# Performance work log

Measured on AMD Instinct MI355X. Metric: run time of the kernel, lower is better.

Reference implementation:

```python
import jax, jax.numpy as jnp
import numpy as np

DIM = 128
HEADS = 4
DH = 32
SCALE = DH ** -0.5


def _ln(x, g, b):
    m = x.mean(-1, keepdims=True)
    v = x.var(-1, keepdims=True)
    return (x - m) / jnp.sqrt(v + 1e-5) * g + b


def setup_inputs() -> dict:
    key = jax.random.key(0)
    ks = jax.random.split(key, 16)
    B, N, H, W, HK, WK = 2, 6, 48, 48, 24, 24
    d, hd = DIM, HEADS * DH
    p = lambda k, s: (jax.random.normal(k, s, jnp.float32) * 0.02)
    return {
        "q": jax.random.normal(ks[0], (B, N, d, H, W), jnp.float32),
        "k": jax.random.normal(ks[1], (B, N, d, HK, WK), jnp.float32),
        "v": jax.random.normal(ks[2], (B, N, d, HK, WK), jnp.float32),
        "skip": jax.random.normal(ks[3], (B, d, H, W), jnp.float32),
        "lnq_g": jnp.ones(d), "lnq_b": jnp.zeros(d),
        "Wq": p(ks[4], (d, hd)), "bq": jnp.zeros(hd),
        "lnk_g": jnp.ones(d), "lnk_b": jnp.zeros(d),
        "Wk": p(ks[5], (d, hd)), "bk": jnp.zeros(hd),
        "lnv_g": jnp.ones(d), "lnv_b": jnp.zeros(d),
        "Wv": p(ks[6], (d, hd)), "bv": jnp.zeros(hd),
        "Wp": p(ks[7], (hd, d)), "bp": jnp.zeros(d),
        "pre_g": jnp.ones(d), "pre_b": jnp.zeros(d),
        "W1": p(ks[8], (d, 2 * d)), "b1": jnp.zeros(2 * d),
        "W2": p(ks[9], (2 * d, d)), "b2": jnp.zeros(d),
        "post_g": jnp.ones(d), "post_b": jnp.zeros(d),
    }


def reference(q, k, v, skip, lnq_g, lnq_b, Wq, bq, lnk_g, lnk_b, Wk, bk,
              lnv_g, lnv_b, Wv, bv, Wp, bp, pre_g, pre_b, W1, b1, W2, b2,
              post_g, post_b):
    B, N, d, H, W = q.shape
    _, _, _, HK, WK = k.shape
    Q, K = H * W, HK * WK
    # b n d H W -> b n (H W) d
    qx = q.transpose(0, 1, 3, 4, 2).reshape(B, N, Q, d)
    kx = k.transpose(0, 1, 3, 4, 2).reshape(B, N, K, d)
    vx = v.transpose(0, 1, 3, 4, 2).reshape(B, N * K, d)
    # norm + linear projections
    qp = _ln(qx, lnq_g, lnq_b) @ Wq + bq  # (B,N,Q,HEADS*DH)
    kp = _ln(kx, lnk_g, lnk_b) @ Wk + bk
    vp = _ln(vx, lnv_g, lnv_b) @ Wv + bv  # (B,N*K,HEADS*DH)
    # split heads: b ... (m d) -> (b m) ... d
    qp = qp.reshape(B, N, Q, HEADS, DH).transpose(0, 3, 1, 2, 4).reshape(B * HEADS, N, Q, DH)
    kp = kp.reshape(B, N, K, HEADS, DH).transpose(0, 3, 1, 2, 4).reshape(B * HEADS, N, K, DH)
    vp = vp.reshape(B, N * K, HEADS, DH).transpose(0, 2, 1, 3).reshape(B * HEADS, N * K, DH)
    # per-view scores, then softmax jointly over (n K)
    scores = SCALE * jnp.einsum('bnqd,bnkd->bnqk', qp, kp)
    scores = scores.transpose(0, 2, 1, 3).reshape(B * HEADS, Q, N * K)
    a = jax.nn.softmax(scores, axis=-1)
    out = jnp.einsum('bqk,bkd->bqd', a, vp)  # (B*HEADS, Q, DH)
    # merge heads: (b m) Q d -> b Q (m d)
    z = out.reshape(B, HEADS, Q, DH).transpose(0, 2, 1, 3).reshape(B, Q, HEADS * DH)
    z = z @ Wp + bp
    z = z + skip.transpose(0, 2, 3, 1).reshape(B, Q, d)
    z = _ln(z, pre_g, pre_b)
    z = z + (jax.nn.gelu(z @ W1 + b1, approximate=False) @ W2 + b2)
    z = _ln(z, post_g, post_b)
    return z.reshape(B, H, W, d).transpose(0, 3, 1, 2)
```

## Files before the change

### kernel.cpp

```cpp
#include <hip/hip_runtime.h>
#include <cmath>

#define B_    2
#define N_    6
#define D_    128
#define Q_    2304
#define K_    576
#define NK_   3456
#define HEADS_ 4
#define DH_   32
#define SCALE_ 0.17677669529663687f

typedef __attribute__((ext_vector_type(8))) short bf16x8;
typedef __attribute__((ext_vector_type(4))) float f32x4;

#if defined(__has_builtin)
#if __has_builtin(__builtin_amdgcn_cvt_pk_bf16_f32)
#define HAS_PK_BF16 1
#endif
#endif

static __device__ __forceinline__ unsigned short f2bf(float f) {
  union { float f; unsigned u; } x; x.f = f;
  unsigned u = x.u + 0x7fffu + ((x.u >> 16) & 1u);
  return (unsigned short)(u >> 16);
}
static __device__ __forceinline__ unsigned pkbf(float a, float b) {
#ifdef HAS_PK_BF16
  typedef __attribute__((ext_vector_type(2))) __bf16 vbf2;
  union { vbf2 v; unsigned u; } cv;
  cv.v = __builtin_amdgcn_cvt_pk_bf16_f32(a, b);
  return cv.u;
#else
  return (unsigned)f2bf(a) | ((unsigned)f2bf(b) << 16);
#endif
}

__global__ __launch_bounds__(256) void k_prep_wt(
    const float* __restrict__ Wq, const float* __restrict__ Wk,
    const float* __restrict__ Wv, const float* __restrict__ Wp,
    const float* __restrict__ W1, const float* __restrict__ W2,
    unsigned short* __restrict__ WTq, unsigned short* __restrict__ WTk,
    unsigned short* __restrict__ WTv, unsigned short* __restrict__ WTp,
    unsigned short* __restrict__ WT1, unsigned short* __restrict__ WT2)
{
  __shared__ float tile[32][33];
  const int wb = blockIdx.x, t = threadIdx.x;
  const float* src; unsigned short* dst; int Kd, J, tl;
  if      (wb < 16) { src = Wq; dst = WTq; Kd = 128; J = 128; tl = wb; }
  else if (wb < 32) { src = Wk; dst = WTk; Kd = 128; J = 128; tl = wb - 16; }
  else if (wb < 48) { src = Wv; dst = WTv; Kd = 128; J = 128; tl = wb - 32; }
  else if (wb < 64) { src = Wp; dst = WTp; Kd = 128; J = 128; tl = wb - 48; }
  else if (wb < 96) { src = W1; dst = WT1; Kd = 128; J = 256; tl = wb - 64; }
  else              { src = W2; dst = WT2; Kd = 256; J = 128; tl = wb - 96; }
  const int njt = J >> 5;
  const int tj = tl % njt, tk = tl / njt;
#pragma unroll
  for (int i = 0; i < 4; ++i) {
    int idx = t + 256 * i;
    int r = idx >> 5, c = idx & 31;
    tile[r][c] = src[(size_t)(tk * 32 + r) * J + tj * 32 + c];
  }
  __syncthreads();
#pragma unroll
  for (int i = 0; i < 2; ++i) {
    int idx = t + 256 * i;
    int rr = idx >> 4, c2 = (idx & 15) << 1;
    *(unsigned*)&dst[(size_t)(tj * 32 + rr) * Kd + tk * 32 + c2] =
        pkbf(tile[c2][rr], tile[c2 + 1][rr]);
  }
}

__global__ __launch_bounds__(256) void k_ln_proj_all(
    const float* __restrict__ qin, const float* __restrict__ kin,
    const float* __restrict__ vin,
    const float* __restrict__ lnq_g, const float* __restrict__ lnq_b,
    const float* __restrict__ lnk_g, const float* __restrict__ lnk_b,
    const float* __restrict__ lnv_g, const float* __restrict__ lnv_b,
    const unsigned short* __restrict__ WTq, const unsigned short* __restrict__ WTk,
    const unsigned short* __restrict__ WTv,
    const float* __restrict__ bq, const float* __restrict__ bk,
    const float* __restrict__ bv,
    unsigned short* __restrict__ QPh, unsigned short* __restrict__ KPh,
    unsigned short* __restrict__ VPTh)
{
  __shared__ float xs[32][132];
  __shared__ unsigned short xh[32][136];
  __shared__ float gs[128], bs[128];
  __shared__ float mu[32], rsd[32];
  const int t = threadIdx.x;
  const int bid = blockIdx.x;

  const float* x; const unsigned short* WT; const float* g; const float* bl;
  const float* bias; int S, blk, mode; float osc;
  if (bid < 864)       { mode = 0; blk = bid;        x = qin; WT = WTq; g = lnq_g; bl = lnq_b; bias = bq; S = Q_; osc = SCALE_; }
  else if (bid < 1080) { mode = 0; blk = bid - 864;  x = kin; WT = WTk; g = lnk_g; bl = lnk_b; bias = bk; S = K_; osc = 1.0f; }
  else                 { mode = 1; blk = bid - 1080; x = vin; WT = WTv; g = lnv_g; bl = lnv_b; bias = bv; S = K_; osc = 1.0f; }
  const int ntile = S >> 5;
  const int o  = blk / ntile;
  const int s0 = (blk % ntile) << 5;

  if (t < 128) { gs[t] = g[t]; bs[t] = bl[t]; }
  const float* xb = x + (size_t)o * 128 * (size_t)S + s0;
#pragma unroll
  for (int i = 0; i < 4; ++i) {
    int idx = t + 256 * i;
    int c = idx >> 3, s4 = (idx & 7) << 2;
    float4 xv = *(const float4*)&xb[(size_t)c * S + s4];
    xs[s4 + 0][c] = xv.x; xs[s4 + 1][c] = xv.y;
    xs[s4 + 2][c] = xv.z; xs[s4 + 3][c] = xv.w;
  }
  __syncthreads();
  {
    int s = t >> 3, l8 = t & 7;
    float sum = 0.f, sq = 0.f;
    for (int c = l8; c < 128; c += 8) { float v = xs[s][c]; sum += v; sq += v * v; }
#pragma unroll
    for (int off = 4; off > 0; off >>= 1) {
      sum += __shfl_down(sum, off, 8);
      sq  += __shfl_down(sq,  off, 8);
    }
    if (l8 == 0) {
      float mth = sum * 0.0078125f;
      float var = sq * 0.0078125f - mth * mth;
      mu[s] = mth; rsd[s] = rsqrtf(var + 1e-5f);
    }
  }
  __syncthreads();
#pragma unroll
  for (int i = 0; i < 8; ++i) {
    int idx = t + 256 * i;
    int s = idx >> 6, c2 = (idx & 63) << 1;
    float y0 = (xs[s][c2]     - mu[s]) * rsd[s] * gs[c2]     + bs[c2];
    float y1 = (xs[s][c2 + 1] - mu[s]) * rsd[s] * gs[c2 + 1] + bs[c2 + 1];
    *(unsigned*)&xh[s][c2] = pkbf(y0, y1);
  }
  __syncthreads();
  const int w = t >> 6, lane = t & 63, quad = lane >> 4, l16 = lane & 15;
  const f32x4 zf = {0.f, 0.f, 0.f, 0.f};
  f32x4 acc[2][2] = {{zf, zf}, {zf, zf}};
#pragma unroll
  for (int kc = 0; kc < 4; ++kc) {
    bf16x8 a0 = *(const bf16x8*)&xh[l16][kc * 32 + quad * 8];
    bf16x8 a1 = *(const bf16x8*)&xh[16 + l16][kc * 32 + quad * 8];
    bf16x8 b0 = *(const bf16x8*)&WT[(size_t)(w * 32 + l16) * 128 + kc * 32 + quad * 8];
    bf16x8 b1 = *(const bf16x8*)&WT[(size_t)(w * 32 + 16 + l16) * 128 + kc * 32 + quad * 8];
    acc[0][0] = __builtin_amdgcn_mfma_f32_16x16x32_bf16(a0, b0, acc[0][0], 0, 0, 0);
    acc[0][1] = __builtin_amdgcn_mfma_f32_16x16x32_bf16(a0, b1, acc[0][1], 0, 0, 0);
    acc[1][0] = __builtin_amdgcn_mfma_f32_16x16x32_bf16(a1, b0, acc[1][0], 0, 0, 0);
    acc[1][1] = __builtin_amdgcn_mfma_f32_16x16x32_bf16(a1, b1, acc[1][1], 0, 0, 0);
  }
  if (mode == 0) {
    unsigned short* outh = (bid < 864) ? QPh : KPh;
    __syncthreads();
#pragma unroll
    for (int mt = 0; mt < 2; ++mt)
#pragma unroll
      for (int nt = 0; nt < 2; ++nt) {
        int col = w * 32 + nt * 16 + l16;
        float bc = bias[col];
#pragma unroll
        for (int r = 0; r < 4; ++r)
          xh[mt * 16 + quad * 4 + r][col] = f2bf((acc[mt][nt][r] + bc) * osc);
      }
    __syncthreads();
#pragma unroll
    for (int i = 0; i < 2; ++i) {
      int s = i * 16 + (t >> 4), c8 = (t & 15) << 3;
      *(uint4*)&outh[((size_t)o * S + s0 + s) * 128 + c8] = *(uint4*)&xh[s][c8];
    }
  } else {
    const int b = o / 6, n = o % 6;
#pragma unroll
    for (int mt = 0; mt < 2; ++mt)
#pragma unroll
      for (int nt = 0; nt < 2; ++nt) {
        int col = w * 32 + nt * 16 + l16;
        int hh = col >> 5, dh = col & 31;
        float bc = bias[col];
        ushort4 pk;
        *(unsigned*)&pk.x = pkbf(acc[mt][nt][0] + bc, acc[mt][nt][1] + bc);
        *(unsigned*)&pk.z = pkbf(acc[mt][nt][2] + bc, acc[mt][nt][3] + bc);
        int s = n * 576 + s0 + mt * 16 + quad * 4;
        *(ushort4*)&VPTh[((size_t)(b * 4 + hh) * 32 + dh) * (size_t)NK_ + s] = pk;
      }
  }
}

__global__ __launch_bounds__(256) void k_attn_mfma(
    const unsigned short* __restrict__ QPh, const unsigned short* __restrict__ KPh,
    const unsigned short* __restrict__ VPTh, float* __restrict__ PO,
    float* __restrict__ Pl)
{
  __shared__ __align__(16) char smem_u[10240];
  unsigned short (*plds)[2][16][40] = (unsigned short (*)[2][16][40])smem_u;
  float (*ol)[16][32] = (float (*)[16][32])smem_u;
  __shared__ float ll[4][2][4][16];
  const int t = threadIdx.x;
  const int w = t >> 6, lane = t & 63;
  const int quad = lane >> 4, l16 = lane & 15;
  const int qt = blockIdx.x % 72;
  const int rest = blockIdx.x / 72;
  const int bhx = rest >> 1, ks = rest & 1;
  const int bb = bhx >> 2, h = bhx & 3;
  const int q0 = qt << 5;

  const unsigned short* vbase = VPTh + (size_t)bhx * 32 * (size_t)NK_;
  const f32x4 zf = {0.f, 0.f, 0.f, 0.f};
  f32x4 o00 = zf, o01 = zf, o10 = zf, o11 = zf;
  float lsum0 = 0.f, lsum1 = 0.f;

  const int m8 = ks * 4 + w;
  int c0 = (108 * m8) >> 3, c1 = (108 * (m8 + 1)) >> 3;

  while (c0 < c1) {
    const int nn = c0 / 18;
    const int cend = min(c1, (nn + 1) * 18);
    const unsigned short* kb = &KPh[((size_t)(bb * 6 + nn) * K_) * 128 + h * 32];
    const unsigned short* qb = &QPh[((size_t)(bb * 6 + nn) * Q_ + q0) * 128 + h * 32];
    bf16x8 qc0 = *(const bf16x8*)&qb[(size_t)l16 * 128 + quad * 8];
    bf16x8 qc1 = *(const bf16x8*)&qb[(size_t)(16 + l16) * 128 + quad * 8];

    int kl = (c0 - nn * 18) << 5;
    bf16x8 kf0 = *(const bf16x8*)&kb[(size_t)(kl + l16) * 128 + quad * 8];
    bf16x8 kf1 = *(const bf16x8*)&kb[(size_t)(kl + 16 + l16) * 128 + quad * 8];
    const unsigned short* vb = vbase + ((size_t)c0 << 5);
    bf16x8 vf0 = *(const bf16x8*)&vb[(size_t)l16 * NK_ + quad * 8];
    bf16x8 vf1 = *(const bf16x8*)&vb[(size_t)(16 + l16) * NK_ + quad * 8];

    for (int kc = c0; kc < cend; ++kc) {
      const int kln = (kc + 1 - nn * 18) << 5;
      bf16x8 nk0 = *(const bf16x8*)&kb[(size_t)(kln + l16) * 128 + quad * 8];
      bf16x8 nk1 = *(const bf16x8*)&kb[(size_t)(kln + 16 + l16) * 128 + quad * 8];
      const unsigned short* vbn = vbase + ((size_t)(kc + 1) << 5);
      bf16x8 nv0 = *(const bf16x8*)&vbn[(size_t)l16 * NK_ + quad * 8];
      bf16x8 nv1 = *(const bf16x8*)&vbn[(size_t)(16 + l16) * NK_ + quad * 8];

      f32x4 s00 = __builtin_amdgcn_mfma_f32_16x16x32_bf16(kf0, qc0, zf, 0, 0, 0);
      f32x4 s01 = __builtin_amdgcn_mfma_f32_16x16x32_bf16(kf1, qc0, zf, 0, 0, 0);
      f32x4 s10 = __builtin_amdgcn_mfma_f32_16x16x32_bf16(kf0, qc1, zf, 0, 0, 0);
      f32x4 s11 = __builtin_amdgcn_mfma_f32_16x16x32_bf16(kf1, qc1, zf, 0, 0, 0);

      float a00 = __expf(fminf(s00.x, 70.f)), a01 = __expf(fminf(s00.y, 70.f));
      float a02 = __expf(fminf(s00.z, 70.f)), a03 = __expf(fminf(s00.w, 70.f));
      float a10 = __expf(fminf(s01.x, 70.f)), a11 = __expf(fminf(s01.y, 70.f));
      float a12 = __expf(fminf(s01.z, 70.f)), a13 = __expf(fminf(s01.w, 70.f));
      lsum0 += (a00 + a01 + a02 + a03) + (a10 + a11 + a12 + a13);
      float b00 = __expf(fminf(s10.x, 70.f)), b01 = __expf(fminf(s10.y, 70.f));
      float b02 = __expf(fminf(s10.z, 70.f)), b03 = __expf(fminf(s10.w, 70.f));
      float b10 = __expf(fminf(s11.x, 70.f)), b11 = __expf(fminf(s11.y, 70.f));
      float b12 = __expf(fminf(s11.z, 70.f)), b13 = __expf(fminf(s11.w, 70.f));
      lsum1 += (b00 + b01 + b02 + b03) + (b10 + b11 + b12 + b13);

      uint2 w0a; w0a.x = pkbf(a00, a01); w0a.y = pkbf(a02, a03);
      uint2 w0b; w0b.x = pkbf(a10, a11); w0b.y = pkbf(a12, a13);
      uint2 w1a; w1a.x = pkbf(b00, b01); w1a.y = pkbf(b02, b03);
      uint2 w1b; w1b.x = pkbf(b10, b11); w1b.y = pkbf(b12, b13);
      *(uint2*)&plds[w][0][l16][quad * 4]      = w0a;
      *(uint2*)&plds[w][0][l16][16 + quad * 4] = w0b;
      *(uint2*)&plds[w][1][l16][quad * 4]      = w1a;
      *(uint2*)&plds[w][1][l16][16 + quad * 4] = w1b;
      bf16x8 pf0 = *(const bf16x8*)&plds[w][0][l16][quad * 8];
      bf16x8 pf1 = *(const bf16x8*)&plds[w][1][l16][quad * 8];

      o00 = __builtin_amdgcn_mfma_f32_16x16x32_bf16(pf0, vf0, o00, 0, 0, 0);
      o01 = __builtin_amdgcn_mfma_f32_16x16x32_bf16(pf0, vf1, o01, 0, 0, 0);
      o10 = __builtin_amdgcn_mfma_f32_16x16x32_bf16(pf1, vf0, o10, 0, 0, 0);
      o11 = __builtin_amdgcn_mfma_f32_16x16x32_bf16(pf1, vf1, o11, 0, 0, 0);

      kf0 = nk0; kf1 = nk1; vf0 = nv0; vf1 = nv1;
    }
    c0 = cend;
  }

  ll[w][0][quad][l16] = lsum0;
  ll[w][1][quad][l16] = lsum1;
#pragma unroll
  for (int tt = 0; tt < 2; ++tt) {
    __syncthreads();
    f32x4 t0 = tt ? o10 : o00;
    f32x4 t1 = tt ? o11 : o01;
#pragma unroll
    for (int r = 0; r < 4; ++r) {
      ol[w][quad * 4 + r][l16]      = t0[r];
      ol[w][quad * 4 + r][16 + l16] = t1[r];
    }
    __syncthreads();
    const int q = t >> 4, i16 = t & 15, dd = i16 << 1;
    float a0 = 0.f, a1 = 0.f;
#pragma unroll
    for (int ww = 0; ww < 4; ++ww) { a0 += ol[ww][q][dd]; a1 += ol[ww][q][dd + 1]; }
    float2 r2; r2.x = a0; r2.y = a1;
    *(float2*)&PO[(((size_t)ks * 8 + bhx) * Q_ + q0 + tt * 16 + q) * 32 + dd] = r2;
    if (i16 == 0) {
      float l = 0.f;
#pragma unroll
      for (int ww = 0; ww < 4; ++ww)
#pragma unroll
        for (int qq = 0; qq < 4; ++qq) l += ll[ww][tt][qq][q];
      Pl[((size_t)ks * 8 + bhx) * Q_ + q0 + tt * 16 + q] = l;
    }
  }
}

__global__ __launch_bounds__(512) void k_tail(
    const float* __restrict__ PO, const float* __restrict__ Pl,
    const unsigned short* __restrict__ WTp, const float* __restrict__ bp,
    const float* __restrict__ skip,
    const float* __restrict__ pre_g, const float* __restrict__ pre_b,
    const unsigned short* __restrict__ WT1, const float* __restrict__ b1,
    const unsigned short* __restrict__ WT2, const float* __restrict__ b2,
    const float* __restrict__ post_g, const float* __restrict__ post_b,
    float* __restrict__ out)
{
  __shared__ float xs[16][132];
  __shared__ unsigned short xh[16][136];
  __shared__ unsigned short hb[16][264];
  __shared__ float g1s[128], b1s[128], g2s[128], b2s[128];
  __shared__ float mu[16], rsd[16];
  const int t = threadIdx.x;
  const int row0 = blockIdx.x << 4;
  const int bb = row0 / Q_, hw0 = row0 % Q_;
  const int w = t >> 6, lane = t & 63, quad = lane >> 4, l16 = lane & 15;
  const f32x4 zf = {0.f, 0.f, 0.f, 0.f};

  if (t < 128) { g1s[t] = pre_g[t]; b1s[t] = pre_b[t]; g2s[t] = post_g[t]; b2s[t] = post_b[t]; }
#pragma unroll
  for (int i = 0; i < 2; ++i) {
    int idx = t + 512 * i;
    int s = idx >> 6, c2 = (idx & 63) << 1;
    int q = hw0 + s;
    int h = c2 >> 5, dh = c2 & 31;
    size_t bq = (size_t)(bb * 4 + h) * Q_ + q;
    size_t i0 = bq * 32 + dh;
    float2 p0 = *(const float2*)&PO[i0];
    float2 p1 = *(const float2*)&PO[589824 + i0];
    float inv = 1.f / (Pl[bq] + Pl[18432 + bq]);
    *(unsigned*)&xh[s][c2] = pkbf((p0.x + p1.x) * inv, (p0.y + p1.y) * inv);
  }
  __syncthreads();
  {
    f32x4 acc = zf;
    const int col = w * 16 + l16;
#pragma unroll
    for (int kc = 0; kc < 4; ++kc) {
      bf16x8 a0 = *(const bf16x8*)&xh[l16][kc * 32 + quad * 8];
      bf16x8 b0 = *(const bf16x8*)&WTp[(size_t)col * 128 + kc * 32 + quad * 8];
      acc = __builtin_amdgcn_mfma_f32_16x16x32_bf16(a0, b0, acc, 0, 0, 0);
    }
    float bc = bp[col];
    float4 sk = *(const float4*)&skip[((size_t)bb * 128 + col) * Q_ + hw0 + quad * 4];
    xs[quad * 4 + 0][col] = acc[0] + bc + sk.x;
    xs[quad * 4 + 1][col] = acc[1] + bc + sk.y;
    xs[quad * 4 + 2][col] = acc[2] + bc + sk.z;
    xs[quad * 4 + 3][col] = acc[3] + bc + sk.w;
  }
  __syncthreads();
  {
    int s = t >> 5, lg = t & 31;
    float sum = 0.f, sq = 0.f;
    for (int c = lg; c < 128; c += 32) { float v = xs[s][c]; sum += v; sq += v * v; }
#pragma unroll
    for (int off = 16; off > 0; off >>= 1) {
      sum += __shfl_down(sum, off, 32);
      sq  += __shfl_down(sq,  off, 32);
    }
    if (lg == 0) {
      float mth = sum * 0.0078125f;
      float var = sq * 0.0078125f - mth * mth;
      mu[s] = mth; rsd[s] = rsqrtf(var + 1e-5f);
    }
  }
  __syncthreads();
#pragma unroll
  for (int i = 0; i < 2; ++i) {
    int idx = t + 512 * i;
    int s = idx >> 6, c2 = (idx & 63) << 1;
    float y0 = (xs[s][c2]     - mu[s]) * rsd[s] * g1s[c2]     + b1s[c2];
    float y1 = (xs[s][c2 + 1] - mu[s]) * rsd[s] * g1s[c2 + 1] + b1s[c2 + 1];
    xs[s][c2] = y0; xs[s][c2 + 1] = y1;
    *(unsigned*)&xh[s][c2] = pkbf(y0, y1);
  }
  __syncthreads();
  {
#pragma unroll
    for (int nt = 0; nt < 2; ++nt) {
      const int col = w * 32 + nt * 16 + l16;
      f32x4 acc = zf;
#pragma unroll
      for (int kc = 0; kc < 4; ++kc) {
        bf16x8 a0 = *(const bf16x8*)&xh[l16][kc * 32 + quad * 8];
        bf16x8 b0 = *(const bf16x8*)&WT1[(size_t)col * 128 + kc * 32 + quad * 8];
        acc = __builtin_amdgcn_mfma_f32_16x16x32_bf16(a0, b0, acc, 0, 0, 0);
      }
      float bc = b1[col];
#pragma unroll
      for (int r = 0; r < 4; ++r) {
        float hx = acc[r] + bc;
        hb[quad * 4 + r][col] =
            f2bf(0.5f * hx * (1.f + erff(hx * 0.7071067811865476f)));
      }
    }
  }
  __syncthreads();
  {
    f32x4 acc = zf;
    const int col = w * 16 + l16;
#pragma unroll
    for (int kc = 0; kc < 8; ++kc) {
      bf16x8 a0 = *(const bf16x8*)&hb[l16][kc * 32 + quad * 8];
      bf16x8 b0 = *(const bf16x8*)&WT2[(size_t)col * 256 + kc * 32 + quad * 8];
      acc = __builtin_amdgcn_mfma_f32_16x16x32_bf16(a0, b0, acc, 0, 0, 0);
    }
    float bc = b2[col];
#pragma unroll
    for (int r = 0; r < 4; ++r) {
      int row = quad * 4 + r;
      xs[row][col] = acc[r] + bc + xs[row][col];
    }
  }
  __syncthreads();
  {
    int s = t >> 5, lg = t & 31;
    float sum = 0.f, sq = 0.f;
    for (int c = lg; c < 128; c += 32) { float v = xs[s][c]; sum += v; sq += v * v; }
#pragma unroll
    for (int off = 16; off > 0; off >>= 1) {
      sum += __shfl_down(sum, off, 32);
      sq  += __shfl_down(sq,  off, 32);
    }
    if (lg == 0) {
      float mth = sum * 0.0078125f;
      float var = sq * 0.0078125f - mth * mth;
      mu[s] = mth; rsd[s] = rsqrtf(var + 1e-5f);
    }
  }
  __syncthreads();
#pragma unroll
  for (int i = 0; i < 4; ++i) {
    int idx = t + 512 * i;
    int s = idx & 15, c = idx >> 4;
    out[(size_t)bb * (128 * (size_t)Q_) + (size_t)c * Q_ + hw0 + s] =
        (xs[s][c] - mu[s]) * rsd[s] * g2s[c] + b2s[c];
  }
}

extern "C" void kernel_launch(void* const* d_in, const int* in_sizes, int n_in,
                              void* d_out, int out_size, void* d_ws, size_t ws_size,
                              hipStream_t stream) {
  const float* q     = (const float*)d_in[0];
  const float* k     = (const float*)d_in[1];
  const float* v     = (const float*)d_in[2];
  const float* skip  = (const float*)d_in[3];
  const float* lnq_g = (const float*)d_in[4];
  const float* lnq_b = (const float*)d_in[5];
  const float* Wq    = (const float*)d_in[6];
  const float* bq    = (const float*)d_in[7];
  const float* lnk_g = (const float*)d_in[8];
  const float* lnk_b = (const float*)d_in[9];
  const float* Wk    = (const float*)d_in[10];
  const float* bk    = (const float*)d_in[11];
  const float* lnv_g = (const float*)d_in[12];
  const float* lnv_b = (const float*)d_in[13];
  const float* Wv    = (const float*)d_in[14];
  const float* bvv   = (const float*)d_in[15];
  const float* Wp    = (const float*)d_in[16];
  const float* bp    = (const float*)d_in[17];
  const float* pre_g = (const float*)d_in[18];
  const float* pre_b = (const float*)d_in[19];
  const float* W1    = (const float*)d_in[20];
  const float* b1    = (const float*)d_in[21];
  const float* W2    = (const float*)d_in[22];
  const float* b2    = (const float*)d_in[23];
  const float* post_g= (const float*)d_in[24];
  const float* post_b= (const float*)d_in[25];
  float* out = (float*)d_out;

  unsigned short* QPh  = (unsigned short*)d_ws;
  unsigned short* KPh  = QPh + 3538944;
  unsigned short* VPTh = KPh + 884736;
  float* PO  = (float*)(VPTh + 884736);
  float* Pl  = PO + 1179648;
  unsigned short* WTq = (unsigned short*)(Pl + 36864);
  unsigned short* WTk = WTq + 16384;
  unsigned short* WTv = WTk + 16384;
  unsigned short* WTp = WTv + 16384;
  unsigned short* WT1 = WTp + 16384;
  unsigned short* WT2 = WT1 + 32768;

  k_prep_wt<<<dim3(128), dim3(256), 0, stream>>>(Wq, Wk, Wv, Wp, W1, W2,
                                                 WTq, WTk, WTv, WTp, WT1, WT2);
  k_ln_proj_all<<<dim3(1296), dim3(256), 0, stream>>>(
      q, k, v, lnq_g, lnq_b, lnk_g, lnk_b, lnv_g, lnv_b,
      WTq, WTk, WTv, bq, bk, bvv, QPh, KPh, VPTh);
  k_attn_mfma<<<dim3(1152), dim3(256), 0, stream>>>(QPh, KPh, VPTh, PO, Pl);
  k_tail<<<dim3(288), dim3(512), 0, stream>>>(PO, Pl, WTp, bp, skip,
                                              pre_g, pre_b, WT1, b1, WT2, b2,
                                              post_g, post_b, out);
}
```

Baseline: 176.9 us.

## Restructure projection and attention kernels with head-major layouts and MFMA row sums

The LN+projection kernel now gives each wave a 16-row tile, with LayerNorm done in registers and the full 128-column output computed per wave, and no block-wide LDS staging. Q and K are stored head-major, and V is stored in 32x32 chunk blocks so attention loads are contiguous. Attention uses 16-query tiles and folds log2(e) into the Q scale so it can use exp2. It computes row sums with an MFMA against a ones vector, software-pipelines the score MFMAs one chunk ahead, and double-buffers the P tile in LDS. The trade-offs are more blocks and halved Q reuse per K/V load, plus the removal of the exp clamp that guarded against overflow.

```diff
diff --git a/kernel.cpp b/kernel.cpp
--- a/kernel.cpp
+++ b/kernel.cpp
@@ -10,6 +10,9 @@
 #define HEADS_ 4
 #define DH_   32
 #define SCALE_ 0.17677669529663687f
+#define SCLOG2E_ 0.25504672615621814f
+#define VCHUNKS_ 108
+#define VCSZ_ (VCHUNKS_*1024)
 
 typedef __attribute__((ext_vector_type(8))) short bf16x8;
 typedef __attribute__((ext_vector_type(4))) float f32x4;
@@ -82,133 +85,130 @@
     const float* __restrict__ bq, const float* __restrict__ bk,
     const float* __restrict__ bv,
     unsigned short* __restrict__ QPh, unsigned short* __restrict__ KPh,
-    unsigned short* __restrict__ VPTh)
+    unsigned short* __restrict__ Vc)
 {
-  __shared__ float xs[32][132];
-  __shared__ unsigned short xh[32][136];
-  __shared__ float gs[128], bs[128];
-  __shared__ float mu[32], rsd[32];
+  __shared__ float wl[4][16][132];
   const int t = threadIdx.x;
-  const int bid = blockIdx.x;
+  const int w = t >> 6, lane = t & 63, quad = lane >> 4, l16 = lane & 15;
+  const int gt = blockIdx.x * 4 + w;
 
   const float* x; const unsigned short* WT; const float* g; const float* bl;
-  const float* bias; int S, blk, mode; float osc;
-  if (bid < 864)       { mode = 0; blk = bid;        x = qin; WT = WTq; g = lnq_g; bl = lnq_b; bias = bq; S = Q_; osc = SCALE_; }
-  else if (bid < 1080) { mode = 0; blk = bid - 864;  x = kin; WT = WTk; g = lnk_g; bl = lnk_b; bias = bk; S = K_; osc = 1.0f; }
-  else                 { mode = 1; blk = bid - 1080; x = vin; WT = WTv; g = lnv_g; bl = lnv_b; bias = bv; S = K_; osc = 1.0f; }
-  const int ntile = S >> 5;
-  const int o  = blk / ntile;
-  const int s0 = (blk % ntile) << 5;
-
-  if (t < 128) { gs[t] = g[t]; bs[t] = bl[t]; }
+  const float* bias; int S, o, s0, mode; float osc;
+  unsigned short* outh = nullptr;
+  if (gt < 1728)      { mode = 0; o = gt / 144;  s0 = (gt % 144) << 4; x = qin; WT = WTq; g = lnq_g; bl = lnq_b; bias = bq; S = Q_; osc = SCLOG2E_; outh = QPh; }
+  else if (gt < 2160) { int kt = gt - 1728; mode = 0; o = kt / 36; s0 = (kt % 36) << 4; x = kin; WT = WTk; g = lnk_g; bl = lnk_b; bias = bk; S = K_; osc = 1.0f; outh = KPh; }
+  else                { int vt = gt - 2160; mode = 1; o = vt / 36; s0 = (vt % 36) << 4; x = vin; WT = WTv; g = lnv_g; bl = lnv_b; bias = bv; S = K_; osc = 1.0f; }
+
   const float* xb = x + (size_t)o * 128 * (size_t)S + s0;
-#pragma unroll
-  for (int i = 0; i < 4; ++i) {
-    int idx = t + 256 * i;
-    int c = idx >> 3, s4 = (idx & 7) << 2;
-    float4 xv = *(const float4*)&xb[(size_t)c * S + s4];
-    xs[s4 + 0][c] = xv.x; xs[s4 + 1][c] = xv.y;
-    xs[s4 + 2][c] = xv.z; xs[s4 + 3][c] = xv.w;
-  }
-  __syncthreads();
-  {
-    int s = t >> 3, l8 = t & 7;
-    float sum = 0.f, sq = 0.f;
-    for (int c = l8; c < 128; c += 8) { float v = xs[s][c]; sum += v; sq += v * v; }
-#pragma unroll
-    for (int off = 4; off > 0; off >>= 1) {
-      sum += __shfl_down(sum, off, 8);
-      sq  += __shfl_down(sq,  off, 8);
-    }
-    if (l8 == 0) {
-      float mth = sum * 0.0078125f;
-      float var = sq * 0.0078125f - mth * mth;
-      mu[s] = mth; rsd[s] = rsqrtf(var + 1e-5f);
-    }
-  }
-  __syncthreads();
-#pragma unroll
-  for (int i = 0; i < 8; ++i) {
-    int idx = t + 256 * i;
-    int s = idx >> 6, c2 = (idx & 63) << 1;
-    float y0 = (xs[s][c2]     - mu[s]) * rsd[s] * gs[c2]     + bs[c2];
-    float y1 = (xs[s][c2 + 1] - mu[s]) * rsd[s] * gs[c2 + 1] + bs[c2 + 1];
-    *(unsigned*)&xh[s][c2] = pkbf(y0, y1);
-  }
-  __syncthreads();
-  const int w = t >> 6, lane = t & 63, quad = lane >> 4, l16 = lane & 15;
+  float xv[4][8];
+#pragma unroll
+  for (int kc = 0; kc < 4; ++kc)
+#pragma unroll
+    for (int j = 0; j < 8; ++j)
+      xv[kc][j] = xb[(size_t)(kc * 32 + quad * 8 + j) * S + l16];
+
+  float sum = 0.f, sq = 0.f;
+#pragma unroll
+  for (int kc = 0; kc < 4; ++kc)
+#pragma unroll
+    for (int j = 0; j < 8; ++j) { float v = xv[kc][j]; sum += v; sq += v * v; }
+  sum += __shfl_xor(sum, 16); sq += __shfl_xor(sq, 16);
+  sum += __shfl_xor(sum, 32); sq += __shfl_xor(sq, 32);
+  const float mean = sum * 0.0078125f;
+  const float rsd = rsqrtf(sq * 0.0078125f - mean * mean + 1e-5f);
+
+  bf16x8 afr[4];
+#pragma unroll
+  for (int kc = 0; kc < 4; ++kc) {
+    float4 g0 = *(const float4*)&g[kc * 32 + quad * 8];
+    float4 g1 = *(const float4*)&g[kc * 32 + quad * 8 + 4];
+    float4 b0 = *(const float4*)&bl[kc * 32 + quad * 8];
+    float4 b1 = *(const float4*)&bl[kc * 32 + quad * 8 + 4];
+    float y[8];
+    y[0] = (xv[kc][0] - mean) * rsd * g0.x + b0.x;
+    y[1] = (xv[kc][1] - mean) * rsd * g0.y + b0.y;
+    y[2] = (xv[kc][2] - mean) * rsd * g0.z + b0.z;
+    y[3] = (xv[kc][3] - mean) * rsd * g0.w + b0.w;
+    y[4] = (xv[kc][4] - mean) * rsd * g1.x + b1.x;
+    y[5] = (xv[kc][5] - mean) * rsd * g1.y + b1.y;
+    y[6] = (xv[kc][6] - mean) * rsd * g1.z + b1.z;
+    y[7] = (xv[kc][7] - mean) * rsd * g1.w + b1.w;
+    unsigned u0 = pkbf(y[0], y[1]), u1 = pkbf(y[2], y[3]);
+    unsigned u2 = pkbf(y[4], y[5]), u3 = pkbf(y[6], y[7]);
+    union { unsigned u[4]; bf16x8 v; } cv;
+    cv.u[0] = u0; cv.u[1] = u1; cv.u[2] = u2; cv.u[3] = u3;
+    afr[kc] = cv.v;
+  }
+
   const f32x4 zf = {0.f, 0.f, 0.f, 0.f};
-  f32x4 acc[2][2] = {{zf, zf}, {zf, zf}};
-#pragma unroll
-  for (int kc = 0; kc < 4; ++kc) {
-    bf16x8 a0 = *(const bf16x8*)&xh[l16][kc * 32 + quad * 8];
-    bf16x8 a1 = *(const bf16x8*)&xh[16 + l16][kc * 32 + quad * 8];
-    bf16x8 b0 = *(const bf16x8*)&WT[(size_t)(w * 32 + l16) * 128 + kc * 32 + quad * 8];
-    bf16x8 b1 = *(const bf16x8*)&WT[(size_t)(w * 32 + 16 + l16) * 128 + kc * 32 + quad * 8];
-    acc[0][0] = __builtin_amdgcn_mfma_f32_16x16x32_bf16(a0, b0, acc[0][0], 0, 0, 0);
-    acc[0][1] = __builtin_amdgcn_mfma_f32_16x16x32_bf16(a0, b1, acc[0][1], 0, 0, 0);
-    acc[1][0] = __builtin_amdgcn_mfma_f32_16x16x32_bf16(a1, b0, acc[1][0], 0, 0, 0);
-    acc[1][1] = __builtin_amdgcn_mfma_f32_16x16x32_bf16(a1, b1, acc[1][1], 0, 0, 0);
-  }
+  f32x4 acc[8] = {zf, zf, zf, zf, zf, zf, zf, zf};
+#pragma unroll
+  for (int ct = 0; ct < 8; ++ct)
+#pragma unroll
+    for (int kc = 0; kc < 4; ++kc) {
+      bf16x8 bf = *(const bf16x8*)&WT[(size_t)(ct * 16 + l16) * 128 + kc * 32 + quad * 8];
+      acc[ct] = __builtin_amdgcn_mfma_f32_16x16x32_bf16(afr[kc], bf, acc[ct], 0, 0, 0);
+    }
+
   if (mode == 0) {
-    unsigned short* outh = (bid < 864) ? QPh : KPh;
-    __syncthreads();
-#pragma unroll
-    for (int mt = 0; mt < 2; ++mt)
-#pragma unroll
-      for (int nt = 0; nt < 2; ++nt) {
-        int col = w * 32 + nt * 16 + l16;
-        float bc = bias[col];
-#pragma unroll
-        for (int r = 0; r < 4; ++r)
-          xh[mt * 16 + quad * 4 + r][col] = f2bf((acc[mt][nt][r] + bc) * osc);
-      }
-    __syncthreads();
-#pragma unroll
-    for (int i = 0; i < 2; ++i) {
-      int s = i * 16 + (t >> 4), c8 = (t & 15) << 3;
-      *(uint4*)&outh[((size_t)o * S + s0 + s) * 128 + c8] = *(uint4*)&xh[s][c8];
-    }
+#pragma unroll
+    for (int ct = 0; ct < 8; ++ct) {
+      float bc = bias[ct * 16 + l16];
+#pragma unroll
+      for (int r = 0; r < 4; ++r)
+        wl[w][quad * 4 + r][ct * 16 + l16] = acc[ct][r] + bc;
+    }
+    unsigned short* dst = outh + ((size_t)(o * 4 + quad) * S + s0 + l16) * 32;
+    unsigned short tmp[32];
+#pragma unroll
+    for (int m = 0; m < 16; ++m) {
+      float v0 = wl[w][l16][quad * 32 + 2 * m];
+      float v1 = wl[w][l16][quad * 32 + 2 * m + 1];
+      *(unsigned*)&tmp[2 * m] = pkbf(v0 * osc, v1 * osc);
+    }
+#pragma unroll
+    for (int m = 0; m < 4; ++m)
+      *(uint4*)&dst[m * 8] = *(uint4*)&tmp[m * 8];
   } else {
     const int b = o / 6, n = o % 6;
 #pragma unroll
-    for (int mt = 0; mt < 2; ++mt)
-#pragma unroll
-      for (int nt = 0; nt < 2; ++nt) {
-        int col = w * 32 + nt * 16 + l16;
-        int hh = col >> 5, dh = col & 31;
-        float bc = bias[col];
-        ushort4 pk;
-        *(unsigned*)&pk.x = pkbf(acc[mt][nt][0] + bc, acc[mt][nt][1] + bc);
-        *(unsigned*)&pk.z = pkbf(acc[mt][nt][2] + bc, acc[mt][nt][3] + bc);
-        int s = n * 576 + s0 + mt * 16 + quad * 4;
-        *(ushort4*)&VPTh[((size_t)(b * 4 + hh) * 32 + dh) * (size_t)NK_ + s] = pk;
-      }
+    for (int ct = 0; ct < 8; ++ct) {
+      int col = ct * 16 + l16, hh = col >> 5, dh = col & 31;
+      float bc = bias[col];
+      int kg = n * 576 + s0 + quad * 4;
+      ushort4 pk;
+      *(unsigned*)&pk.x = pkbf(acc[ct][0] + bc, acc[ct][1] + bc);
+      *(unsigned*)&pk.z = pkbf(acc[ct][2] + bc, acc[ct][3] + bc);
+      *(ushort4*)&Vc[(size_t)(b * 4 + hh) * VCSZ_ + (kg >> 5) * 1024 + dh * 32 + (kg & 31)] = pk;
+    }
   }
 }
 
 __global__ __launch_bounds__(256) void k_attn_mfma(
     const unsigned short* __restrict__ QPh, const unsigned short* __restrict__ KPh,
-    const unsigned short* __restrict__ VPTh, float* __restrict__ PO,
+    const unsigned short* __restrict__ Vc, float* __restrict__ PO,
     float* __restrict__ Pl)
 {
   __shared__ __align__(16) char smem_u[10240];
-  unsigned short (*plds)[2][16][40] = (unsigned short (*)[2][16][40])smem_u;
+  typedef unsigned short plds_t[2][16][40];
+  plds_t* plds = (plds_t*)smem_u;
   float (*ol)[16][32] = (float (*)[16][32])smem_u;
-  __shared__ float ll[4][2][4][16];
+  __shared__ float ll[4][16];
   const int t = threadIdx.x;
   const int w = t >> 6, lane = t & 63;
   const int quad = lane >> 4, l16 = lane & 15;
-  const int qt = blockIdx.x % 72;
-  const int rest = blockIdx.x / 72;
+  const int qt = blockIdx.x % 144;
+  const int rest = blockIdx.x / 144;
   const int bhx = rest >> 1, ks = rest & 1;
   const int bb = bhx >> 2, h = bhx & 3;
-  const int q0 = qt << 5;
-
-  const unsigned short* vbase = VPTh + (size_t)bhx * 32 * (size_t)NK_;
+  const int q0 = qt << 4;
+
+  const unsigned short* vc = Vc + (size_t)bhx * VCSZ_;
   const f32x4 zf = {0.f, 0.f, 0.f, 0.f};
-  f32x4 o00 = zf, o01 = zf, o10 = zf, o11 = zf;
-  float lsum0 = 0.f, lsum1 = 0.f;
+  const short onebf = (short)0x3F80;
+  const bf16x8 onesb = {onebf, onebf, onebf, onebf, onebf, onebf, onebf, onebf};
+  f32x4 o0 = zf, o1 = zf, lacc = zf;
+  int buf = 0;
 
   const int m8 = ks * 4 + w;
   int c0 = (108 * m8) >> 3, c1 = (108 * (m8 + 1)) >> 3;
@@ -216,89 +216,75 @@
   while (c0 < c1) {
     const int nn = c0 / 18;
     const int cend = min(c1, (nn + 1) * 18);
-    const unsigned short* kb = &KPh[((size_t)(bb * 6 + nn) * K_) * 128 + h * 32];
-    const unsigned short* qb = &QPh[((size_t)(bb * 6 + nn) * Q_ + q0) * 128 + h * 32];
-    bf16x8 qc0 = *(const bf16x8*)&qb[(size_t)l16 * 128 + quad * 8];
-    bf16x8 qc1 = *(const bf16x8*)&qb[(size_t)(16 + l16) * 128 + quad * 8];
-
-    int kl = (c0 - nn * 18) << 5;
-    bf16x8 kf0 = *(const bf16x8*)&kb[(size_t)(kl + l16) * 128 + quad * 8];
-    bf16x8 kf1 = *(const bf16x8*)&kb[(size_t)(kl + 16 + l16) * 128 + quad * 8];
-    const unsigned short* vb = vbase + ((size_t)c0 << 5);
-    bf16x8 vf0 = *(const bf16x8*)&vb[(size_t)l16 * NK_ + quad * 8];
-    bf16x8 vf1 = *(const bf16x8*)&vb[(size_t)(16 + l16) * NK_ + quad * 8];
-
+    const unsigned short* kb = KPh + (size_t)((bb * 6 + nn) * 4 + h) * K_ * 32;
+    const unsigned short* qb = QPh + (size_t)((bb * 6 + nn) * 4 + h) * Q_ * 32 + (size_t)q0 * 32;
+    bf16x8 qc = *(const bf16x8*)&qb[l16 * 32 + quad * 8];
+
+    const int kl0 = (c0 - nn * 18) << 5;
+    bf16x8 v0a = *(const bf16x8*)&vc[(size_t)c0 * 1024 + l16 * 32 + quad * 8];
+    bf16x8 v0b = *(const bf16x8*)&vc[(size_t)c0 * 1024 + (16 + l16) * 32 + quad * 8];
+    bf16x8 k0a = *(const bf16x8*)&kb[(size_t)(kl0 + l16) * 32 + quad * 8];
+    bf16x8 k0b = *(const bf16x8*)&kb[(size_t)(kl0 + 16 + l16) * 32 + quad * 8];
+    bf16x8 k1a = *(const bf16x8*)&kb[(size_t)(kl0 + 32 + l16) * 32 + quad * 8];
+    bf16x8 k1b = *(const bf16x8*)&kb[(size_t)(kl0 + 48 + l16) * 32 + quad * 8];
+    bf16x8 v1a = *(const bf16x8*)&vc[(size_t)(c0 + 1) * 1024 + l16 * 32 + quad * 8];
+    bf16x8 v1b = *(const bf16x8*)&vc[(size_t)(c0 + 1) * 1024 + (16 + l16) * 32 + quad * 8];
+    f32x4 s0 = __builtin_amdgcn_mfma_f32_16x16x32_bf16(k0a, qc, zf, 0, 0, 0);
+    f32x4 s1 = __builtin_amdgcn_mfma_f32_16x16x32_bf16(k0b, qc, zf, 0, 0, 0);
+
+#pragma unroll 2
     for (int kc = c0; kc < cend; ++kc) {
-      const int kln = (kc + 1 - nn * 18) << 5;
-      bf16x8 nk0 = *(const bf16x8*)&kb[(size_t)(kln + l16) * 128 + quad * 8];
-      bf16x8 nk1 = *(const bf16x8*)&kb[(size_t)(kln + 16 + l16) * 128 + quad * 8];
-      const unsigned short* vbn = vbase + ((size_t)(kc + 1) << 5);
-      bf16x8 nv0 = *(const bf16x8*)&vbn[(size_t)l16 * NK_ + quad * 8];
-      bf16x8 nv1 = *(const bf16x8*)&vbn[(size_t)(16 + l16) * NK_ + quad * 8];
-
-      f32x4 s00 = __builtin_amdgcn_mfma_f32_16x16x32_bf16(kf0, qc0, zf, 0, 0, 0);
-      f32x4 s01 = __builtin_amdgcn_mfma_f32_16x16x32_bf16(kf1, qc0, zf, 0, 0, 0);
-      f32x4 s10 = __builtin_amdgcn_mfma_f32_16x16x32_bf16(kf0, qc1, zf, 0, 0, 0);
-      f32x4 s11 = __builtin_amdgcn_mfma_f32_16x16x32_bf16(kf1, qc1, zf, 0, 0, 0);
-
-      float a00 = __expf(fminf(s00.x, 70.f)), a01 = __expf(fminf(s00.y, 70.f));
-      float a02 = __expf(fminf(s00.z, 70.f)), a03 = __expf(fminf(s00.w, 70.f));
-      float a10 = __expf(fminf(s01.x, 70.f)), a11 = __expf(fminf(s01.y, 70.f));
-      float a12 = __expf(fminf(s01.z, 70.f)), a13 = __expf(fminf(s01.w, 70.f));
-      lsum0 += (a00 + a01 + a02 + a03) + (a10 + a11 + a12 + a13);
-      float b00 = __expf(fminf(s10.x, 70.f)), b01 = __expf(fminf(s10.y, 70.f));
-      float b02 = __expf(fminf(s10.z, 70.f)), b03 = __expf(fminf(s10.w, 70.f));
-      float b10 = __expf(fminf(s11.x, 70.f)), b11 = __expf(fminf(s11.y, 70.f));
-      float b12 = __expf(fminf(s11.z, 70.f)), b13 = __expf(fminf(s11.w, 70.f));
-      lsum1 += (b00 + b01 + b02 + b03) + (b10 + b11 + b12 + b13);
-
-      uint2 w0a; w0a.x = pkbf(a00, a01); w0a.y = pkbf(a02, a03);
-      uint2 w0b; w0b.x = pkbf(a10, a11); w0b.y = pkbf(a12, a13);
-      uint2 w1a; w1a.x = pkbf(b00, b01); w1a.y = pkbf(b02, b03);
-      uint2 w1b; w1b.x = pkbf(b10, b11); w1b.y = pkbf(b12, b13);
-      *(uint2*)&plds[w][0][l16][quad * 4]      = w0a;
-      *(uint2*)&plds[w][0][l16][16 + quad * 4] = w0b;
-      *(uint2*)&plds[w][1][l16][quad * 4]      = w1a;
-      *(uint2*)&plds[w][1][l16][16 + quad * 4] = w1b;
-      bf16x8 pf0 = *(const bf16x8*)&plds[w][0][l16][quad * 8];
-      bf16x8 pf1 = *(const bf16x8*)&plds[w][1][l16][quad * 8];
-
-      o00 = __builtin_amdgcn_mfma_f32_16x16x32_bf16(pf0, vf0, o00, 0, 0, 0);
-      o01 = __builtin_amdgcn_mfma_f32_16x16x32_bf16(pf0, vf1, o01, 0, 0, 0);
-      o10 = __builtin_amdgcn_mfma_f32_16x16x32_bf16(pf1, vf0, o10, 0, 0, 0);
-      o11 = __builtin_amdgcn_mfma_f32_16x16x32_bf16(pf1, vf1, o11, 0, 0, 0);
-
-      kf0 = nk0; kf1 = nk1; vf0 = nv0; vf1 = nv1;
+      const int kl2 = (kc + 2 - nn * 18) << 5;
+      bf16x8 k2a = *(const bf16x8*)&kb[(size_t)(kl2 + l16) * 32 + quad * 8];
+      bf16x8 k2b = *(const bf16x8*)&kb[(size_t)(kl2 + 16 + l16) * 32 + quad * 8];
+      bf16x8 v2a = *(const bf16x8*)&vc[(size_t)(kc + 2) * 1024 + l16 * 32 + quad * 8];
+      bf16x8 v2b = *(const bf16x8*)&vc[(size_t)(kc + 2) * 1024 + (16 + l16) * 32 + quad * 8];
+
+      float p0 = exp2f(s0.x), p1 = exp2f(s0.y), p2 = exp2f(s0.z), p3 = exp2f(s0.w);
+      float p4 = exp2f(s1.x), p5 = exp2f(s1.y), p6 = exp2f(s1.z), p7 = exp2f(s1.w);
+      uint2 wa; wa.x = pkbf(p0, p1); wa.y = pkbf(p2, p3);
+      uint2 wb2; wb2.x = pkbf(p4, p5); wb2.y = pkbf(p6, p7);
+      *(uint2*)&plds[w][buf][l16][quad * 4]      = wa;
+      *(uint2*)&plds[w][buf][l16][16 + quad * 4] = wb2;
+      bf16x8 pf = *(const bf16x8*)&plds[w][buf][l16][quad * 8];
+
+      o0   = __builtin_amdgcn_mfma_f32_16x16x32_bf16(pf, v0a, o0, 0, 0, 0);
+      o1   = __builtin_amdgcn_mfma_f32_16x16x32_bf16(pf, v0b, o1, 0, 0, 0);
+      lacc = __builtin_amdgcn_mfma_f32_16x16x32_bf16(pf, onesb, lacc, 0, 0, 0);
+
+      s0 = __builtin_amdgcn_mfma_f32_16x16x32_bf16(k1a, qc, zf, 0, 0, 0);
+      s1 = __builtin_amdgcn_mfma_f32_16x16x32_bf16(k1b, qc, zf, 0, 0, 0);
+
+      v0a = v1a; v0b = v1b;
+      k1a = k2a; k1b = k2b; v1a = v2a; v1b = v2b;
+      buf ^= 1;
     }
     c0 = cend;
   }
 
-  ll[w][0][quad][l16] = lsum0;
-  ll[w][1][quad][l16] = lsum1;
-#pragma unroll
-  for (int tt = 0; tt < 2; ++tt) {
-    __syncthreads();
-    f32x4 t0 = tt ? o10 : o00;
-    f32x4 t1 = tt ? o11 : o01;
-#pragma unroll
-    for (int r = 0; r < 4; ++r) {
-      ol[w][quad * 4 + r][l16]      = t0[r];
-      ol[w][quad * 4 + r][16 + l16] = t1[r];
-    }
-    __syncthreads();
+  if (l16 == 0) {
+#pragma unroll
+    for (int r = 0; r < 4; ++r) ll[w][quad * 4 + r] = lacc[r];
+  }
+  __syncthreads();
+#pragma unroll
+  for (int r = 0; r < 4; ++r) {
+    ol[w][quad * 4 + r][l16]      = o0[r];
+    ol[w][quad * 4 + r][16 + l16] = o1[r];
+  }
+  __syncthreads();
+  {
     const int q = t >> 4, i16 = t & 15, dd = i16 << 1;
     float a0 = 0.f, a1 = 0.f;
 #pragma unroll
     for (int ww = 0; ww < 4; ++ww) { a0 += ol[ww][q][dd]; a1 += ol[ww][q][dd + 1]; }
     float2 r2; r2.x = a0; r2.y = a1;
-    *(float2*)&PO[(((size_t)ks * 8 + bhx) * Q_ + q0 + tt * 16 + q) * 32 + dd] = r2;
+    *(float2*)&PO[(((size_t)ks * 8 + bhx) * Q_ + q0 + q) * 32 + dd] = r2;
     if (i16 == 0) {
       float l = 0.f;
 #pragma unroll
-      for (int ww = 0; ww < 4; ++ww)
-#pragma unroll
-        for (int qq = 0; qq < 4; ++qq) l += ll[ww][tt][qq][q];
-      Pl[((size_t)ks * 8 + bhx) * Q_ + q0 + tt * 16 + q] = l;
+      for (int ww = 0; ww < 4; ++ww) l += ll[ww][q];
+      Pl[((size_t)ks * 8 + bhx) * Q_ + q0 + q] = l;
     }
   }
 }
@@ -476,10 +462,10 @@
   const float* post_b= (const float*)d_in[25];
   float* out = (float*)d_out;
 
-  unsigned short* QPh  = (unsigned short*)d_ws;
-  unsigned short* KPh  = QPh + 3538944;
-  unsigned short* VPTh = KPh + 884736;
-  float* PO  = (float*)(VPTh + 884736);
+  unsigned short* QPh = (unsigned short*)d_ws;
+  unsigned short* KPh = QPh + 3538944;
+  unsigned short* Vc  = KPh + 884736;
+  float* PO  = (float*)(Vc + 884736);
   float* Pl  = PO + 1179648;
   unsigned short* WTq = (unsigned short*)(Pl + 36864);
   unsigned short* WTk = WTq + 16384;
@@ -490,10 +476,10 @@
 
   k_prep_wt<<<dim3(128), dim3(256), 0, stream>>>(Wq, Wk, Wv, Wp, W1, W2,
                                                  WTq, WTk, WTv, WTp, WT1, WT2);
-  k_ln_proj_all<<<dim3(1296), dim3(256), 0, stream>>>(
+  k_ln_proj_all<<<dim3(648), dim3(256), 0, stream>>>(
       q, k, v, lnq_g, lnq_b, lnk_g, lnk_b, lnv_g, lnv_b,
-      WTq, WTk, WTv, bq, bk, bvv, QPh, KPh, VPTh);
-  k_attn_mfma<<<dim3(1152), dim3(256), 0, stream>>>(QPh, KPh, VPTh, PO, Pl);
+      WTq, WTk, WTv, bq, bk, bvv, QPh, KPh, Vc);
+  k_attn_mfma<<<dim3(2304), dim3(256), 0, stream>>>(QPh, KPh, Vc, PO, Pl);
   k_tail<<<dim3(288), dim3(512), 0, stream>>>(PO, Pl, WTp, bp, skip,
                                               pre_g, pre_b, WT1, b1, WT2, b2,
                                               post_g, post_b, out);
```

New measurement: 186.3 us. 1.05x slower.
